# Kernel tuning notes

Measured on AMD Instinct MI355X. Metric: run time of the kernel, lower is better.

Reference implementation:

```python
import jax, jax.numpy as jnp
import numpy as np

N = 50000      # nodes
E = 800000     # edges (before self-loops)
F_IN = 256     # num_features
H = 4          # heads
C = 64         # hidden_channels
HC = H * C     # 256
L = 2          # n_layers
G = 128        # num graphs
DENSE = 64     # dense_nhid
NCLS = 2       # num_classes
NEG_SLOPE = 0.2
BN_EPS = 1e-5


def setup_inputs() -> dict:
    key = jax.random.key(0)
    ks = jax.random.split(key, 16)
    s = 0.1
    inp = {}
    inp['x'] = jax.random.normal(ks[0], (N, F_IN), jnp.float32)
    inp['edge_index'] = jax.random.randint(ks[1], (2, E), 0, N, dtype=jnp.int32)
    inp['batch'] = jnp.sort(jax.random.randint(ks[2], (N,), 0, G, dtype=jnp.int32))
    # conv1 (GATConv: lin weight [in, H*C], att vectors [H, C], bias [H*C])
    inp['W1'] = jax.random.normal(ks[3], (F_IN, HC), jnp.float32) * s
    inp['as1'] = jax.random.normal(ks[4], (H, C), jnp.float32) * s
    inp['ad1'] = jax.random.normal(ks[5], (H, C), jnp.float32) * s
    inp['b1'] = jnp.zeros((HC,), jnp.float32)
    # stacked params for the L inner conv layers + their BatchNorms
    inp['Wl'] = jax.random.normal(ks[6], (L, HC, HC), jnp.float32) * s
    inp['asl'] = jax.random.normal(ks[7], (L, H, C), jnp.float32) * s
    inp['adl'] = jax.random.normal(ks[8], (L, H, C), jnp.float32) * s
    inp['bl'] = jnp.zeros((L, HC), jnp.float32)
    inp['bng'] = jnp.ones((L, HC), jnp.float32)
    inp['bnb'] = jnp.zeros((L, HC), jnp.float32)
    # bn1 + MLP head
    inp['bn1g'] = jnp.ones((HC,), jnp.float32)
    inp['bn1b'] = jnp.zeros((HC,), jnp.float32)
    inp['lin1W'] = jax.random.normal(ks[9], (HC, DENSE), jnp.float32) * s
    inp['lin1b'] = jnp.zeros((DENSE,), jnp.float32)
    inp['lin2W'] = jax.random.normal(ks[10], (DENSE, DENSE), jnp.float32) * s
    inp['lin2b'] = jnp.zeros((DENSE,), jnp.float32)
    inp['lin3W'] = jax.random.normal(ks[11], (DENSE, NCLS), jnp.float32) * s
    inp['lin3b'] = jnp.zeros((NCLS,), jnp.float32)
    return inp


def _gat(x, src, dst, W, a_src, a_dst, b):
    # GATConv: h_j = W x_j; e_ij = LeakyReLU(a_src.h_j + a_dst.h_i);
    # alpha = softmax over incoming edges of node i; out_i = sum_j alpha*h_j (concat heads) + bias
    h = (x @ W).reshape(-1, H, C)                       # [N, H, C]
    es = jnp.sum(h * a_src, axis=-1)                    # [N, H]
    ed = jnp.sum(h * a_dst, axis=-1)                    # [N, H]
    e = jax.nn.leaky_relu(es[src] + ed[dst], NEG_SLOPE) # [E2, H]
    m = jax.ops.segment_max(e, dst, num_segments=N)
    ex = jnp.exp(e - m[dst])
    ssum = jax.ops.segment_sum(ex, dst, num_segments=N)
    alpha = ex / (ssum[dst] + 1e-16)                    # [E2, H]
    agg = jax.ops.segment_sum(h[src] * alpha[:, :, None], dst, num_segments=N)
    return agg.reshape(-1, HC) + b


def _bn(x, g, b):
    # BatchNorm1d in training mode (biased batch variance)
    mu = jnp.mean(x, axis=0)
    var = jnp.mean((x - mu) ** 2, axis=0)
    return (x - mu) / jnp.sqrt(var + BN_EPS) * g + b


def reference(x, edge_index, batch, W1, as1, ad1, b1, Wl, asl, adl, bl, bng, bnb,
              bn1g, bn1b, lin1W, lin1b, lin2W, lin2b, lin3W, lin3b):
    loops = jnp.arange(N, dtype=edge_index.dtype)
    src = jnp.concatenate([edge_index[0], loops])  # GATConv adds self-loops
    dst = jnp.concatenate([edge_index[1], loops])
    h = jax.nn.relu(_gat(x, src, dst, W1, as1, ad1, b1))
    for i in range(L):
        h = jax.nn.relu(_bn(_gat(h, src, dst, Wl[i], asl[i], adl[i], bl[i]), bng[i], bnb[i]))
    cnt = jax.ops.segment_sum(jnp.ones((N,), h.dtype), batch, num_segments=G)
    pooled = jax.ops.segment_sum(h, batch, num_segments=G) / jnp.maximum(cnt, 1.0)[:, None]
    z = _bn(pooled, bn1g, bn1b)  # dropout is identity in eval
    z = jax.nn.relu(z @ lin1W + lin1b)
    z = jax.nn.relu(z @ lin2W + lin2b)
    z = jax.nn.relu(z @ lin3W + lin3b)
    out = jax.nn.softmax(z, axis=1)
    return (out, pooled)
```

## Files before the change

### kernel.cpp

```cpp
#include <hip/hip_runtime.h>

#define N_NODES 50000
#define E_EDGES 800000
#define E2 (E_EDGES + N_NODES)
#define HC 256
#define NHEAD 4
#define GG 128
#define DENSE 64
#define NCLS 2
#define BN_EPS 1e-5f
#define NEG_SLOPE 0.2f
#define NEG_BIG -1e30f

typedef __attribute__((ext_vector_type(8))) short bf16x8;
typedef __attribute__((ext_vector_type(4))) float f32x4;

__device__ __forceinline__ unsigned short f2bf(float f) {
    unsigned int u = __float_as_uint(f);
    u = (u + 0x7FFFu + ((u >> 16) & 1u)) >> 16;
    return (unsigned short)u;
}
__device__ __forceinline__ float bf2f(unsigned short h) {
    return __uint_as_float(((unsigned int)h) << 16);
}
__device__ __forceinline__ float lrelu(float e) {
    return (e >= 0.f) ? e : NEG_SLOPE * e;
}
__device__ __forceinline__ void accum8(float acc[8], uint4 v, float w) {
    acc[0] = fmaf(w, __uint_as_float(v.x << 16), acc[0]);
    acc[1] = fmaf(w, __uint_as_float(v.x & 0xffff0000u), acc[1]);
    acc[2] = fmaf(w, __uint_as_float(v.y << 16), acc[2]);
    acc[3] = fmaf(w, __uint_as_float(v.y & 0xffff0000u), acc[3]);
    acc[4] = fmaf(w, __uint_as_float(v.z << 16), acc[4]);
    acc[5] = fmaf(w, __uint_as_float(v.z & 0xffff0000u), acc[5]);
    acc[6] = fmaf(w, __uint_as_float(v.w << 16), acc[6]);
    acc[7] = fmaf(w, __uint_as_float(v.w & 0xffff0000u), acc[7]);
}

__global__ __launch_bounds__(256) void convert_bf16_kernel(const float* __restrict__ in,
                                                           unsigned short* __restrict__ out,
                                                           int n8) {
    int i = blockIdx.x * blockDim.x + threadIdx.x;
    if (i >= n8) return;
    const float4* p = reinterpret_cast<const float4*>(in + (size_t)i * 8);
    float4 a = p[0], b = p[1];
    ushort4 lo = make_ushort4(f2bf(a.x), f2bf(a.y), f2bf(a.z), f2bf(a.w));
    ushort4 hi = make_ushort4(f2bf(b.x), f2bf(b.y), f2bf(b.z), f2bf(b.w));
    ushort4* q = reinterpret_cast<ushort4*>(out + (size_t)i * 8);
    q[0] = lo; q[1] = hi;
}

__global__ __launch_bounds__(64) void pack_b_kernel(const float* __restrict__ W,
                                                    unsigned short* __restrict__ Bpk) {
    int l = threadIdx.x;
    int g = blockIdx.x;
    int ks = g >> 4, ct = g & 15;
    int col = ct * 16 + (l & 15);
    int k0 = ks * 32 + (l >> 4) * 8;
    unsigned short v[8];
#pragma unroll
    for (int j = 0; j < 8; ++j) v[j] = f2bf(W[(size_t)(k0 + j) * HC + col]);
    ushort4* q = reinterpret_cast<ushort4*>(Bpk + ((size_t)g * 64 + l) * 8);
    q[0] = make_ushort4(v[0], v[1], v[2], v[3]);
    q[1] = make_ushort4(v[4], v[5], v[6], v[7]);
}

__global__ __launch_bounds__(256) void gemm_mfma_kernel(const unsigned short* __restrict__ A,
                                                        const unsigned short* __restrict__ Bpk,
                                                        const float* __restrict__ prm,
                                                        unsigned short* __restrict__ C, int M) {
    __shared__ unsigned short As[64 * 256];
    int tid = threadIdx.x;
    int lane = tid & 63, wid = tid >> 6;
    int row0 = blockIdx.x * 64;
#pragma unroll
    for (int i = 0; i < 8; ++i) {
        int idx = tid + i * 256;
        int row = idx >> 5, c16 = idx & 31;
        int grow = row0 + row;
        uint4 v = make_uint4(0u, 0u, 0u, 0u);
        if (grow < M) v = *reinterpret_cast<const uint4*>(A + (size_t)grow * HC + c16 * 8);
        if (prm) {
            int ch = c16 * 8;
            const float4 s0 = *reinterpret_cast<const float4*>(prm + ch);
            const float4 s1 = *reinterpret_cast<const float4*>(prm + ch + 4);
            const float4 t0 = *reinterpret_cast<const float4*>(prm + HC + ch);
            const float4 t1 = *reinterpret_cast<const float4*>(prm + HC + ch + 4);
            float f0 = fmaxf(fmaf(__uint_as_float(v.x << 16),          s0.x, t0.x), 0.f);
            float f1 = fmaxf(fmaf(__uint_as_float(v.x & 0xffff0000u),  s0.y, t0.y), 0.f);
            float f2 = fmaxf(fmaf(__uint_as_float(v.y << 16),          s0.z, t0.z), 0.f);
            float f3 = fmaxf(fmaf(__uint_as_float(v.y & 0xffff0000u),  s0.w, t0.w), 0.f);
            float f4 = fmaxf(fmaf(__uint_as_float(v.z << 16),          s1.x, t1.x), 0.f);
            float f5 = fmaxf(fmaf(__uint_as_float(v.z & 0xffff0000u),  s1.y, t1.y), 0.f);
            float f6 = fmaxf(fmaf(__uint_as_float(v.w << 16),          s1.z, t1.z), 0.f);
            float f7 = fmaxf(fmaf(__uint_as_float(v.w & 0xffff0000u),  s1.w, t1.w), 0.f);
            v.x = (unsigned int)f2bf(f0) | ((unsigned int)f2bf(f1) << 16);
            v.y = (unsigned int)f2bf(f2) | ((unsigned int)f2bf(f3) << 16);
            v.z = (unsigned int)f2bf(f4) | ((unsigned int)f2bf(f5) << 16);
            v.w = (unsigned int)f2bf(f6) | ((unsigned int)f2bf(f7) << 16);
        }
        int byteoff = row * 512 + c16 * 16;
        byteoff ^= (row & 7) << 4;
        *reinterpret_cast<uint4*>((char*)As + byteoff) = v;
    }
    __syncthreads();

    f32x4 acc[16];
#pragma unroll
    for (int ct = 0; ct < 16; ++ct) acc[ct] = (f32x4){0.f, 0.f, 0.f, 0.f};

    int mrow = wid * 16 + (lane & 15);
#pragma unroll
    for (int ks = 0; ks < 8; ++ks) {
        int abyte = mrow * 512 + ks * 64 + (lane >> 4) * 16;
        abyte ^= (mrow & 7) << 4;
        bf16x8 a = *reinterpret_cast<const bf16x8*>((char*)As + abyte);
        const unsigned short* bp = Bpk + ((size_t)(ks * 16) * 512 + lane * 8);
#pragma unroll
        for (int ct = 0; ct < 16; ++ct) {
            bf16x8 b = *reinterpret_cast<const bf16x8*>(bp + (size_t)ct * 512);
            acc[ct] = __builtin_amdgcn_mfma_f32_16x16x32_bf16(a, b, acc[ct], 0, 0, 0);
        }
    }
    int crow0 = row0 + wid * 16 + (lane >> 4) * 4;
    int ccol = lane & 15;
#pragma unroll
    for (int ct = 0; ct < 16; ++ct) {
#pragma unroll
        for (int r = 0; r < 4; ++r) {
            int grow = crow0 + r;
            if (grow < M) C[(size_t)grow * HC + ct * 16 + ccol] = f2bf(acc[ct][r]);
        }
    }
}

__global__ __launch_bounds__(256) void esed_kernel(const unsigned short* __restrict__ h,
                                                   const float* __restrict__ avs,
                                                   const float* __restrict__ avd,
                                                   float* __restrict__ es, float* __restrict__ ed) {
    int tid = threadIdx.x;
    int lane = tid & 63, wid = tid >> 6;
    int node = blockIdx.x * 4 + wid;
    if (node >= N_NODES) return;
    int ch0 = lane * 4;
    ushort4 hv = *reinterpret_cast<const ushort4*>(h + (size_t)node * HC + ch0);
    float4 sa = *reinterpret_cast<const float4*>(avs + ch0);
    float4 da = *reinterpret_cast<const float4*>(avd + ch0);
    float h0 = bf2f(hv.x), h1 = bf2f(hv.y), h2 = bf2f(hv.z), h3 = bf2f(hv.w);
    float vs = h0 * sa.x + h1 * sa.y + h2 * sa.z + h3 * sa.w;
    float vd = h0 * da.x + h1 * da.y + h2 * da.z + h3 * da.w;
#pragma unroll
    for (int m = 1; m < 16; m <<= 1) {
        vs += __shfl_xor(vs, m, 64);
        vd += __shfl_xor(vd, m, 64);
    }
    if ((lane & 15) == 0) {
        es[node * NHEAD + (lane >> 4)] = vs;
        ed[node * NHEAD + (lane >> 4)] = vd;
    }
}

__global__ void init_deg_kernel(int* __restrict__ deg) {
    int i = blockIdx.x * blockDim.x + threadIdx.x;
    if (i < N_NODES) deg[i] = 1;
}
__global__ void count_edges_kernel(const int* __restrict__ dst, int* __restrict__ deg) {
    int i = blockIdx.x * blockDim.x + threadIdx.x;
    if (i < E_EDGES) atomicAdd(&deg[dst[i]], 1);
}
__global__ __launch_bounds__(1024) void scan1_kernel(const int* __restrict__ deg,
                                                     int* __restrict__ rs, int* __restrict__ bsum) {
    __shared__ int wsum[16];
    int t = threadIdx.x, lane = t & 63, wid = t >> 6;
    int i = blockIdx.x * 1024 + t;
    int v = (i < N_NODES) ? deg[i] : 0;
    int x = v;
#pragma unroll
    for (int off = 1; off < 64; off <<= 1) {
        int y = __shfl_up(x, off, 64);
        if (lane >= off) x += y;
    }
    if (lane == 63) wsum[wid] = x;
    __syncthreads();
    if (wid == 0) {
        int s = (lane < 16) ? wsum[lane] : 0;
#pragma unroll
        for (int off = 1; off < 16; off <<= 1) {
            int y = __shfl_up(s, off, 64);
            if (lane >= off) s += y;
        }
        if (lane < 16) wsum[lane] = s;
    }
    __syncthreads();
    int woff = wid ? wsum[wid - 1] : 0;
    if (i <= N_NODES) rs[i] = woff + x - v;
    if (t == 1023) bsum[blockIdx.x] = wsum[15];
}
__global__ void scan2_kernel(int* __restrict__ bsum, int nb) {
    int l = threadIdx.x;
    int v = (l < nb) ? bsum[l] : 0;
    int x = v;
#pragma unroll
    for (int off = 1; off < 64; off <<= 1) {
        int y = __shfl_up(x, off, 64);
        if (l >= off) x += y;
    }
    if (l < nb) bsum[l] = x - v;
}
__global__ void scan3_kernel(int* __restrict__ rs, const int* __restrict__ bsum,
                             int* __restrict__ cursor, int* __restrict__ csr) {
    int i = blockIdx.x * blockDim.x + threadIdx.x;
    if (i <= N_NODES) {
        int v = rs[i] + bsum[i >> 10];
        rs[i] = v;
        if (i < N_NODES) {
            csr[v] = i;
            cursor[i] = v + 1;
        }
    }
}
__global__ void scatter_edges_kernel(const int* __restrict__ src, const int* __restrict__ dst,
                                     int* __restrict__ cursor, int* __restrict__ csr) {
    int i = blockIdx.x * blockDim.x + threadIdx.x;
    if (i < E_EDGES) {
        int pos = atomicAdd(&cursor[dst[i]], 1);
        csr[pos] = src[i];
    }
}

__global__ __launch_bounds__(256) void smprep_kernel(const float* __restrict__ es,
                                                     const float* __restrict__ ed,
                                                     const int* __restrict__ rs,
                                                     const int* __restrict__ csr,
                                                     float* __restrict__ alpha) {
    int tid = threadIdx.x;
    int lane = tid & 63, wid = tid >> 6;
    int node = blockIdx.x * 4 + wid;
    if (node >= N_NODES) return;
    int head = lane >> 4, slot = lane & 15;
    float edn = ed[node * NHEAD + head];
    int beg = rs[node], end = rs[node + 1];
    float m = NEG_BIG, s = 0.f;
    for (int i = beg + slot; i < end; i += 16) {
        float e = lrelu(es[csr[i] * NHEAD + head] + edn);
        alpha[(size_t)i * NHEAD + head] = e;
        float mn = fmaxf(m, e);
        s = s * __expf(m - mn) + __expf(e - mn);
        m = mn;
    }
#pragma unroll
    for (int off = 1; off < 16; off <<= 1) {
        float mo = __shfl_xor(m, off, 64);
        float so = __shfl_xor(s, off, 64);
        float mn = fmaxf(m, mo);
        s = s * __expf(m - mn) + so * __expf(mo - mn);
        m = mn;
    }
    float inv = 1.f / (s + 1e-16f);
    for (int i = beg + slot; i < end; i += 16) {
        float e = alpha[(size_t)i * NHEAD + head];
        alpha[(size_t)i * NHEAD + head] = __expf(e - m) * inv;
    }
}

__global__ __launch_bounds__(256) void gat_agg_kernel(const unsigned short* __restrict__ hlin,
                                                      const float* __restrict__ alpha,
                                                      const int* __restrict__ rs,
                                                      const int* __restrict__ csr,
                                                      const float* __restrict__ bias,
                                                      unsigned short* __restrict__ out, int do_relu) {
    int tid = threadIdx.x;
    int lane = tid & 63, wid = tid >> 6;
    int node = blockIdx.x * 8 + wid * 2 + (lane >> 5);
    int hl = lane & 31;
    int ch0 = hl * 8;
    int head = hl >> 3;
    bool valid = node < N_NODES;
    int beg = valid ? rs[node] : 0;
    int end = valid ? rs[node + 1] : 0;
    float acc[8] = {};
    int idx = beg;
    for (; idx + 8 <= end; idx += 8) {
        int si[8]; float pi[8];
#pragma unroll
        for (int j = 0; j < 8; ++j) {
            si[j] = csr[idx + j];
            pi[j] = alpha[(size_t)(idx + j) * NHEAD + head];
        }
        uint4 v[8];
#pragma unroll
        for (int j = 0; j < 8; ++j)
            v[j] = *reinterpret_cast<const uint4*>(hlin + (size_t)si[j] * HC + ch0);
#pragma unroll
        for (int j = 0; j < 8; ++j) accum8(acc, v[j], pi[j]);
    }
    if (idx + 4 <= end) {
        int s0 = csr[idx], s1 = csr[idx + 1], s2 = csr[idx + 2], s3 = csr[idx + 3];
        float p0 = alpha[(size_t)idx * NHEAD + head];
        float p1 = alpha[(size_t)(idx + 1) * NHEAD + head];
        float p2 = alpha[(size_t)(idx + 2) * NHEAD + head];
        float p3 = alpha[(size_t)(idx + 3) * NHEAD + head];
        uint4 v0 = *reinterpret_cast<const uint4*>(hlin + (size_t)s0 * HC + ch0);
        uint4 v1 = *reinterpret_cast<const uint4*>(hlin + (size_t)s1 * HC + ch0);
        uint4 v2 = *reinterpret_cast<const uint4*>(hlin + (size_t)s2 * HC + ch0);
        uint4 v3 = *reinterpret_cast<const uint4*>(hlin + (size_t)s3 * HC + ch0);
        accum8(acc, v0, p0);
        accum8(acc, v1, p1);
        accum8(acc, v2, p2);
        accum8(acc, v3, p3);
        idx += 4;
    }
    for (; idx < end; ++idx) {
        int s0 = csr[idx];
        float p0 = alpha[(size_t)idx * NHEAD + head];
        uint4 v0 = *reinterpret_cast<const uint4*>(hlin + (size_t)s0 * HC + ch0);
        accum8(acc, v0, p0);
    }
    if (!valid) return;
    const float4 bva = *reinterpret_cast<const float4*>(bias + ch0);
    const float4 bvb = *reinterpret_cast<const float4*>(bias + ch0 + 4);
    float o[8];
    o[0] = acc[0] + bva.x; o[1] = acc[1] + bva.y; o[2] = acc[2] + bva.z; o[3] = acc[3] + bva.w;
    o[4] = acc[4] + bvb.x; o[5] = acc[5] + bvb.y; o[6] = acc[6] + bvb.z; o[7] = acc[7] + bvb.w;
    if (do_relu) {
#pragma unroll
        for (int j = 0; j < 8; ++j) o[j] = fmaxf(o[j], 0.f);
    }
    uint4 w;
    w.x = (unsigned int)f2bf(o[0]) | ((unsigned int)f2bf(o[1]) << 16);
    w.y = (unsigned int)f2bf(o[2]) | ((unsigned int)f2bf(o[3]) << 16);
    w.z = (unsigned int)f2bf(o[4]) | ((unsigned int)f2bf(o[5]) << 16);
    w.w = (unsigned int)f2bf(o[6]) | ((unsigned int)f2bf(o[7]) << 16);
    *reinterpret_cast<uint4*>(out + (size_t)node * HC + ch0) = w;
}

#define BN_RPB 49
__global__ __launch_bounds__(256) void bn_stats_kernel(const unsigned short* __restrict__ x,
                                                       float* __restrict__ sums) {
    __shared__ float lds[8][512];
    int tid = threadIdx.x;
    int c = tid & 31;
    int rt = tid >> 5;
    int r0 = blockIdx.x * BN_RPB;
    int r1 = min(N_NODES, r0 + BN_RPB);
    int ch = c * 8;
    float s[8] = {}, s2[8] = {};
    for (int r = r0 + rt; r < r1; r += 8) {
        const ushort4* p = reinterpret_cast<const ushort4*>(x + (size_t)r * HC + ch);
        ushort4 va = p[0], vb = p[1];
        unsigned short in[8] = {va.x, va.y, va.z, va.w, vb.x, vb.y, vb.z, vb.w};
#pragma unroll
        for (int j = 0; j < 8; ++j) {
            float v = bf2f(in[j]);
            s[j] += v; s2[j] += v * v;
        }
    }
#pragma unroll
    for (int j = 0; j < 8; ++j) {
        lds[rt][ch + j] = s[j];
        lds[rt][256 + ch + j] = s2[j];
    }
    __syncthreads();
#pragma unroll
    for (int e = tid; e < 512; e += 256) {
        float v = 0.f;
#pragma unroll
        for (int r = 0; r < 8; ++r) v += lds[r][e];
        atomicAdd(&sums[e], v);
    }
}
__global__ void bn_finalize_kernel(const float* __restrict__ sums, const float* __restrict__ g,
                                   const float* __restrict__ b, float* __restrict__ prm) {
    int t = threadIdx.x;
    float mean = sums[t] / (float)N_NODES;
    float var = sums[HC + t] / (float)N_NODES - mean * mean;
    var = fmaxf(var, 0.f);
    float scale = g[t] * rsqrtf(var + BN_EPS);
    prm[t] = scale;
    prm[HC + t] = b[t] - mean * scale;
}

__global__ __launch_bounds__(GG) void graph_ub_kernel(const int* __restrict__ batch,
                                                      int* __restrict__ ub) {
    int g = threadIdx.x;
    int lo = 0, hi = N_NODES;
    while (lo < hi) {
        int mid = (lo + hi) >> 1;
        if (batch[mid] <= g) lo = mid + 1; else hi = mid;
    }
    ub[g] = lo;
}
#define POOL_RPB 32
__global__ __launch_bounds__(256) void pool_kernel(const unsigned short* __restrict__ h,
                                                   const float* __restrict__ prm,
                                                   const int* __restrict__ batch,
                                                   float* __restrict__ psum) {
    int tid = threadIdx.x;
    int ct = tid & 63;
    int rt = tid >> 6;
    int r0 = blockIdx.x * POOL_RPB;
    int r1 = min(N_NODES, r0 + POOL_RPB);
    int ch = ct * 4;
    const float4 sc = *reinterpret_cast<const float4*>(prm + ch);
    const float4 sh = *reinterpret_cast<const float4*>(prm + HC + ch);
    float a0 = 0.f, a1 = 0.f, a2 = 0.f, a3 = 0.f;
    int gcur = -1;
    for (int r = r0 + rt; r < r1; r += 4) {
        int g = batch[r];
        if (g != gcur) {
            if (gcur >= 0) {
                atomicAdd(&psum[gcur * HC + ch + 0], a0);
                atomicAdd(&psum[gcur * HC + ch + 1], a1);
                atomicAdd(&psum[gcur * HC + ch + 2], a2);
                atomicAdd(&psum[gcur * HC + ch + 3], a3);
            }
            a0 = a1 = a2 = a3 = 0.f; gcur = g;
        }
        ushort4 hv = *reinterpret_cast<const ushort4*>(h + (size_t)r * HC + ch);
        a0 += fmaxf(fmaf(bf2f(hv.x), sc.x, sh.x), 0.f);
        a1 += fmaxf(fmaf(bf2f(hv.y), sc.y, sh.y), 0.f);
        a2 += fmaxf(fmaf(bf2f(hv.z), sc.z, sh.z), 0.f);
        a3 += fmaxf(fmaf(bf2f(hv.w), sc.w, sh.w), 0.f);
    }
    if (gcur >= 0) {
        atomicAdd(&psum[gcur * HC + ch + 0], a0);
        atomicAdd(&psum[gcur * HC + ch + 1], a1);
        atomicAdd(&psum[gcur * HC + ch + 2], a2);
        atomicAdd(&psum[gcur * HC + ch + 3], a3);
    }
}
__global__ void pool_fin_kernel(const float* __restrict__ psum, const int* __restrict__ ub,
                                float* __restrict__ pooled) {
    int g = blockIdx.x, t = threadIdx.x;
    int c = ub[g] - (g > 0 ? ub[g - 1] : 0);
    float cf = fmaxf((float)c, 1.f);
    pooled[g * HC + t] = psum[g * HC + t] / cf;
}

__global__ __launch_bounds__(256) void bn_head_kernel(const float* __restrict__ pooled,
                                                      const float* __restrict__ g,
                                                      const float* __restrict__ b,
                                                      float* __restrict__ z) {
    int t = threadIdx.x;
    float s = 0.f, s2 = 0.f;
    for (int r = 0; r < GG; ++r) {
        float v = pooled[r * HC + t];
        s += v; s2 += v * v;
    }
    float mean = s / (float)GG;
    float var = fmaxf(s2 / (float)GG - mean * mean, 0.f);
    float scale = g[t] * rsqrtf(var + BN_EPS);
    float shift = b[t] - mean * scale;
    for (int r = 0; r < GG; ++r)
        z[r * HC + t] = pooled[r * HC + t] * scale + shift;
}
__global__ __launch_bounds__(64) void lin_relu_kernel(const float* __restrict__ X,
                                                      const float* __restrict__ W,
                                                      const float* __restrict__ b,
                                                      float* __restrict__ Y, int K) {
    __shared__ float xr[256];
    int r = blockIdx.x, t = threadIdx.x;
    for (int k = t; k < K; k += 64) xr[k] = X[r * K + k];
    __syncthreads();
    float a = b[t];
    for (int k = 0; k < K; ++k) a += xr[k] * W[k * DENSE + t];
    Y[r * DENSE + t] = fmaxf(a, 0.f);
}
__global__ __launch_bounds__(128) void lin3_softmax_kernel(const float* __restrict__ X,
                                                           const float* __restrict__ W,
                                                           const float* __restrict__ b,
                                                           float* __restrict__ out) {
    int r = threadIdx.x;
    const float* xr = X + r * DENSE;
    float o0 = b[0], o1 = b[1];
    for (int k = 0; k < DENSE; ++k) {
        o0 += xr[k] * W[k * NCLS + 0];
        o1 += xr[k] * W[k * NCLS + 1];
    }
    o0 = fmaxf(o0, 0.f); o1 = fmaxf(o1, 0.f);
    float mx = fmaxf(o0, o1);
    float e0 = __expf(o0 - mx), e1 = __expf(o1 - mx);
    float inv = 1.f / (e0 + e1);
    out[r * NCLS + 0] = e0 * inv;
    out[r * NCLS + 1] = e1 * inv;
}

extern "C" void kernel_launch(void* const* d_in, const int* in_sizes, int n_in,
                              void* d_out, int out_size, void* d_ws, size_t ws_size,
                              hipStream_t stream) {
    const float* x     = (const float*)d_in[0];
    const int*   ei    = (const int*)d_in[1];
    const int*   srcp  = ei;
    const int*   dstp  = ei + E_EDGES;
    const int*   batch = (const int*)d_in[2];
    const float* W1    = (const float*)d_in[3];
    const float* as1   = (const float*)d_in[4];
    const float* ad1   = (const float*)d_in[5];
    const float* b1    = (const float*)d_in[6];
    const float* Wl    = (const float*)d_in[7];
    const float* asl   = (const float*)d_in[8];
    const float* adl   = (const float*)d_in[9];
    const float* bl    = (const float*)d_in[10];
    const float* bng   = (const float*)d_in[11];
    const float* bnb   = (const float*)d_in[12];
    const float* bn1g  = (const float*)d_in[13];
    const float* bn1b  = (const float*)d_in[14];
    const float* l1W   = (const float*)d_in[15];
    const float* l1b   = (const float*)d_in[16];
    const float* l2W   = (const float*)d_in[17];
    const float* l2b   = (const float*)d_in[18];
    const float* l3W   = (const float*)d_in[19];
    const float* l3b   = (const float*)d_in[20];

    float* outp   = (float*)d_out;
    float* pooled = outp + GG * NCLS;

    char* w = (char*)d_ws;
    auto alloc = [&](size_t bytes) -> void* {
        void* p = (void*)w;
        w += (bytes + 255) & ~(size_t)255;
        return p;
    };
    unsigned short* xb  = (unsigned short*)alloc(sizeof(short) * (size_t)N_NODES * HC);
    unsigned short* h0  = (unsigned short*)alloc(sizeof(short) * (size_t)N_NODES * HC);
    unsigned short* h1  = (unsigned short*)alloc(sizeof(short) * (size_t)N_NODES * HC);
    unsigned short* h2  = (unsigned short*)alloc(sizeof(short) * (size_t)N_NODES * HC);
    unsigned short* Bpk = (unsigned short*)alloc(sizeof(short) * 3 * 128 * 64 * 8);
    float* es     = (float*)alloc(sizeof(float) * (size_t)N_NODES * NHEAD);
    float* ed     = (float*)alloc(sizeof(float) * (size_t)N_NODES * NHEAD);
    float* alpha  = (float*)alloc(sizeof(float) * (size_t)E2 * NHEAD);
    int*   rs     = (int*)alloc(sizeof(int) * (N_NODES + 1));
    int*   deg    = (int*)alloc(sizeof(int) * N_NODES);
    int*   csr    = (int*)alloc(sizeof(int) * E2);
    int*   bsum   = (int*)alloc(sizeof(int) * 64);
    float* bnsums = (float*)alloc(sizeof(float) * 2 * HC);
    float* bnprm  = (float*)alloc(sizeof(float) * 2 * HC);
    float* psum   = (float*)alloc(sizeof(float) * GG * HC);
    int*   ub     = (int*)alloc(sizeof(int) * GG);
    float* z0     = (float*)alloc(sizeof(float) * GG * HC);
    float* z1     = (float*)alloc(sizeof(float) * GG * DENSE);
    float* z2     = (float*)alloc(sizeof(float) * GG * DENSE);

    const int nblk_nodes = (N_NODES + 255) / 256;
    const int nblk_edges = (E_EDGES + 255) / 256;
    const int nblk_wave4 = (N_NODES + 3) / 4;
    const int nblk_wave8 = (N_NODES + 7) / 8;
    const int nscan = (N_NODES + 1023) / 1024;
    const int nblk_bn   = (N_NODES + BN_RPB - 1) / BN_RPB;
    const int nblk_pool = (N_NODES + POOL_RPB - 1) / POOL_RPB;

    pack_b_kernel<<<128, 64, 0, stream>>>(W1, Bpk);
    pack_b_kernel<<<128, 64, 0, stream>>>(Wl, Bpk + 128 * 64 * 8);
    pack_b_kernel<<<128, 64, 0, stream>>>(Wl + (size_t)HC * HC, Bpk + 2 * 128 * 64 * 8);
    convert_bf16_kernel<<<(N_NODES * HC / 8 + 255) / 256, 256, 0, stream>>>(x, xb, N_NODES * HC / 8);

    init_deg_kernel<<<nblk_nodes, 256, 0, stream>>>(deg);
    count_edges_kernel<<<nblk_edges, 256, 0, stream>>>(dstp, deg);
    scan1_kernel<<<nscan, 1024, 0, stream>>>(deg, rs, bsum);
    scan2_kernel<<<1, 64, 0, stream>>>(bsum, nscan);
    scan3_kernel<<<(N_NODES + 256) / 256, 256, 0, stream>>>(rs, bsum, deg, csr);
    scatter_edges_kernel<<<nblk_edges, 256, 0, stream>>>(srcp, dstp, deg, csr);

    const int ggrid = (N_NODES + 63) / 64;

    gemm_mfma_kernel<<<ggrid, 256, 0, stream>>>(xb, Bpk, nullptr, h1, N_NODES);
    esed_kernel<<<nblk_wave4, 256, 0, stream>>>(h1, as1, ad1, es, ed);
    smprep_kernel<<<nblk_wave4, 256, 0, stream>>>(es, ed, rs, csr, alpha);
    gat_agg_kernel<<<nblk_wave8, 256, 0, stream>>>(h1, alpha, rs, csr, b1, h0, 1);

    gemm_mfma_kernel<<<ggrid, 256, 0, stream>>>(h0, Bpk + 128 * 64 * 8, nullptr, h1, N_NODES);
    esed_kernel<<<nblk_wave4, 256, 0, stream>>>(h1, asl, adl, es, ed);
    smprep_kernel<<<nblk_wave4, 256, 0, stream>>>(es, ed, rs, csr, alpha);
    gat_agg_kernel<<<nblk_wave8, 256, 0, stream>>>(h1, alpha, rs, csr, bl, h2, 0);
    hipMemsetAsync(bnsums, 0, sizeof(float) * 2 * HC, stream);
    bn_stats_kernel<<<nblk_bn, 256, 0, stream>>>(h2, bnsums);
    bn_finalize_kernel<<<1, 256, 0, stream>>>(bnsums, bng, bnb, bnprm);

    gemm_mfma_kernel<<<ggrid, 256, 0, stream>>>(h2, Bpk + 2 * 128 * 64 * 8, bnprm, h1, N_NODES);
    esed_kernel<<<nblk_wave4, 256, 0, stream>>>(h1, asl + HC, adl + HC, es, ed);
    smprep_kernel<<<nblk_wave4, 256, 0, stream>>>(es, ed, rs, csr, alpha);
    gat_agg_kernel<<<nblk_wave8, 256, 0, stream>>>(h1, alpha, rs, csr, bl + HC, h2, 0);
    hipMemsetAsync(bnsums, 0, sizeof(float) * 2 * HC, stream);
    bn_stats_kernel<<<nblk_bn, 256, 0, stream>>>(h2, bnsums);
    bn_finalize_kernel<<<1, 256, 0, stream>>>(bnsums, bng + HC, bnb + HC, bnprm);

    hipMemsetAsync(psum, 0, sizeof(float) * GG * HC, stream);
    graph_ub_kernel<<<1, GG, 0, stream>>>(batch, ub);
    pool_kernel<<<nblk_pool, 256, 0, stream>>>(h2, bnprm, batch, psum);
    pool_fin_kernel<<<GG, HC, 0, stream>>>(psum, ub, pooled);

    bn_head_kernel<<<1, HC, 0, stream>>>(pooled, bn1g, bn1b, z0);
    lin_relu_kernel<<<GG, 64, 0, stream>>>(z0, l1W, l1b, z1, HC);
    lin_relu_kernel<<<GG, 64, 0, stream>>>(z1, l2W, l2b, z2, DENSE);
    lin3_softmax_kernel<<<1, GG, 0, stream>>>(z2, l3W, l3b, outp);
}
```

Measured before the change: 607.0 us.

## Fuse input conversion and attention scores into GEMM, merge small kernels

The fp32-to-bf16 conversion of x now happens in the first GEMM's A-tile load, and the per-node attention dot products (es/ed) are computed in the GEMM epilogue from fp32 accumulators. This drops the convert and esed kernels and one full read of h per layer. The three weight-pack launches become one, and the graph upper-bound kernel is folded into pool_fin as a per-block binary search. The gather loop in gat_agg is cut from 8-wide to 4-wide unrolling, which lowers register pressure but also reduces memory-level parallelism. The es/ed values now come from unrounded accumulators rather than bf16-rounded h, a small numeric difference.

```diff
diff --git a/kernel.cpp b/kernel.cpp
--- a/kernel.cpp
+++ b/kernel.cpp
@@ -37,38 +37,33 @@
     acc[7] = fmaf(w, __uint_as_float(v.w & 0xffff0000u), acc[7]);
 }
 
-__global__ __launch_bounds__(256) void convert_bf16_kernel(const float* __restrict__ in,
-                                                           unsigned short* __restrict__ out,
-                                                           int n8) {
-    int i = blockIdx.x * blockDim.x + threadIdx.x;
-    if (i >= n8) return;
-    const float4* p = reinterpret_cast<const float4*>(in + (size_t)i * 8);
-    float4 a = p[0], b = p[1];
-    ushort4 lo = make_ushort4(f2bf(a.x), f2bf(a.y), f2bf(a.z), f2bf(a.w));
-    ushort4 hi = make_ushort4(f2bf(b.x), f2bf(b.y), f2bf(b.z), f2bf(b.w));
-    ushort4* q = reinterpret_cast<ushort4*>(out + (size_t)i * 8);
-    q[0] = lo; q[1] = hi;
-}
-
-__global__ __launch_bounds__(64) void pack_b_kernel(const float* __restrict__ W,
+__global__ __launch_bounds__(64) void pack_b_kernel(const float* __restrict__ W1,
+                                                    const float* __restrict__ Wl,
                                                     unsigned short* __restrict__ Bpk) {
     int l = threadIdx.x;
-    int g = blockIdx.x;
+    int mat = blockIdx.x >> 7;
+    int g = blockIdx.x & 127;
+    const float* W = (mat == 0) ? W1 : Wl + (size_t)(mat - 1) * HC * HC;
     int ks = g >> 4, ct = g & 15;
     int col = ct * 16 + (l & 15);
     int k0 = ks * 32 + (l >> 4) * 8;
     unsigned short v[8];
 #pragma unroll
     for (int j = 0; j < 8; ++j) v[j] = f2bf(W[(size_t)(k0 + j) * HC + col]);
-    ushort4* q = reinterpret_cast<ushort4*>(Bpk + ((size_t)g * 64 + l) * 8);
+    ushort4* q = reinterpret_cast<ushort4*>(Bpk + ((size_t)mat * 128 * 512) + ((size_t)g * 64 + l) * 8);
     q[0] = make_ushort4(v[0], v[1], v[2], v[3]);
     q[1] = make_ushort4(v[4], v[5], v[6], v[7]);
 }
 
 __global__ __launch_bounds__(256) void gemm_mfma_kernel(const unsigned short* __restrict__ A,
+                                                        const float* __restrict__ A32,
                                                         const unsigned short* __restrict__ Bpk,
                                                         const float* __restrict__ prm,
-                                                        unsigned short* __restrict__ C, int M) {
+                                                        const float* __restrict__ avs,
+                                                        const float* __restrict__ avd,
+                                                        unsigned short* __restrict__ C,
+                                                        float* __restrict__ es,
+                                                        float* __restrict__ ed, int M) {
     __shared__ unsigned short As[64 * 256];
     int tid = threadIdx.x;
     int lane = tid & 63, wid = tid >> 6;
@@ -79,25 +74,36 @@
         int row = idx >> 5, c16 = idx & 31;
         int grow = row0 + row;
         uint4 v = make_uint4(0u, 0u, 0u, 0u);
-        if (grow < M) v = *reinterpret_cast<const uint4*>(A + (size_t)grow * HC + c16 * 8);
-        if (prm) {
-            int ch = c16 * 8;
-            const float4 s0 = *reinterpret_cast<const float4*>(prm + ch);
-            const float4 s1 = *reinterpret_cast<const float4*>(prm + ch + 4);
-            const float4 t0 = *reinterpret_cast<const float4*>(prm + HC + ch);
-            const float4 t1 = *reinterpret_cast<const float4*>(prm + HC + ch + 4);
-            float f0 = fmaxf(fmaf(__uint_as_float(v.x << 16),          s0.x, t0.x), 0.f);
-            float f1 = fmaxf(fmaf(__uint_as_float(v.x & 0xffff0000u),  s0.y, t0.y), 0.f);
-            float f2 = fmaxf(fmaf(__uint_as_float(v.y << 16),          s0.z, t0.z), 0.f);
-            float f3 = fmaxf(fmaf(__uint_as_float(v.y & 0xffff0000u),  s0.w, t0.w), 0.f);
-            float f4 = fmaxf(fmaf(__uint_as_float(v.z << 16),          s1.x, t1.x), 0.f);
-            float f5 = fmaxf(fmaf(__uint_as_float(v.z & 0xffff0000u),  s1.y, t1.y), 0.f);
-            float f6 = fmaxf(fmaf(__uint_as_float(v.w << 16),          s1.z, t1.z), 0.f);
-            float f7 = fmaxf(fmaf(__uint_as_float(v.w & 0xffff0000u),  s1.w, t1.w), 0.f);
-            v.x = (unsigned int)f2bf(f0) | ((unsigned int)f2bf(f1) << 16);
-            v.y = (unsigned int)f2bf(f2) | ((unsigned int)f2bf(f3) << 16);
-            v.z = (unsigned int)f2bf(f4) | ((unsigned int)f2bf(f5) << 16);
-            v.w = (unsigned int)f2bf(f6) | ((unsigned int)f2bf(f7) << 16);
+        if (A32) {
+            if (grow < M) {
+                const float4* p = reinterpret_cast<const float4*>(A32 + (size_t)grow * HC + c16 * 8);
+                float4 a = p[0], b = p[1];
+                v.x = (unsigned int)f2bf(a.x) | ((unsigned int)f2bf(a.y) << 16);
+                v.y = (unsigned int)f2bf(a.z) | ((unsigned int)f2bf(a.w) << 16);
+                v.z = (unsigned int)f2bf(b.x) | ((unsigned int)f2bf(b.y) << 16);
+                v.w = (unsigned int)f2bf(b.z) | ((unsigned int)f2bf(b.w) << 16);
+            }
+        } else {
+            if (grow < M) v = *reinterpret_cast<const uint4*>(A + (size_t)grow * HC + c16 * 8);
+            if (prm) {
+                int ch = c16 * 8;
+                const float4 s0 = *reinterpret_cast<const float4*>(prm + ch);
+                const float4 s1 = *reinterpret_cast<const float4*>(prm + ch + 4);
+                const float4 t0 = *reinterpret_cast<const float4*>(prm + HC + ch);
+                const float4 t1 = *reinterpret_cast<const float4*>(prm + HC + ch + 4);
+                float f0 = fmaxf(fmaf(__uint_as_float(v.x << 16),          s0.x, t0.x), 0.f);
+                float f1 = fmaxf(fmaf(__uint_as_float(v.x & 0xffff0000u),  s0.y, t0.y), 0.f);
+                float f2 = fmaxf(fmaf(__uint_as_float(v.y << 16),          s0.z, t0.z), 0.f);
+                float f3 = fmaxf(fmaf(__uint_as_float(v.y & 0xffff0000u),  s0.w, t0.w), 0.f);
+                float f4 = fmaxf(fmaf(__uint_as_float(v.z << 16),          s1.x, t1.x), 0.f);
+                float f5 = fmaxf(fmaf(__uint_as_float(v.z & 0xffff0000u),  s1.y, t1.y), 0.f);
+                float f6 = fmaxf(fmaf(__uint_as_float(v.w << 16),          s1.z, t1.z), 0.f);
+                float f7 = fmaxf(fmaf(__uint_as_float(v.w & 0xffff0000u),  s1.w, t1.w), 0.f);
+                v.x = (unsigned int)f2bf(f0) | ((unsigned int)f2bf(f1) << 16);
+                v.y = (unsigned int)f2bf(f2) | ((unsigned int)f2bf(f3) << 16);
+                v.z = (unsigned int)f2bf(f4) | ((unsigned int)f2bf(f5) << 16);
+                v.w = (unsigned int)f2bf(f6) | ((unsigned int)f2bf(f7) << 16);
+            }
         }
         int byteoff = row * 512 + c16 * 16;
         byteoff ^= (row & 7) << 4;
@@ -132,31 +138,34 @@
             if (grow < M) C[(size_t)grow * HC + ct * 16 + ccol] = f2bf(acc[ct][r]);
         }
     }
-}
-
-__global__ __launch_bounds__(256) void esed_kernel(const unsigned short* __restrict__ h,
-                                                   const float* __restrict__ avs,
-                                                   const float* __restrict__ avd,
-                                                   float* __restrict__ es, float* __restrict__ ed) {
-    int tid = threadIdx.x;
-    int lane = tid & 63, wid = tid >> 6;
-    int node = blockIdx.x * 4 + wid;
-    if (node >= N_NODES) return;
-    int ch0 = lane * 4;
-    ushort4 hv = *reinterpret_cast<const ushort4*>(h + (size_t)node * HC + ch0);
-    float4 sa = *reinterpret_cast<const float4*>(avs + ch0);
-    float4 da = *reinterpret_cast<const float4*>(avd + ch0);
-    float h0 = bf2f(hv.x), h1 = bf2f(hv.y), h2 = bf2f(hv.z), h3 = bf2f(hv.w);
-    float vs = h0 * sa.x + h1 * sa.y + h2 * sa.z + h3 * sa.w;
-    float vd = h0 * da.x + h1 * da.y + h2 * da.z + h3 * da.w;
-#pragma unroll
-    for (int m = 1; m < 16; m <<= 1) {
-        vs += __shfl_xor(vs, m, 64);
-        vd += __shfl_xor(vd, m, 64);
-    }
-    if ((lane & 15) == 0) {
-        es[node * NHEAD + (lane >> 4)] = vs;
-        ed[node * NHEAD + (lane >> 4)] = vd;
+    float avsv[16], advv[16];
+#pragma unroll
+    for (int ct = 0; ct < 16; ++ct) {
+        avsv[ct] = avs[ct * 16 + ccol];
+        advv[ct] = avd[ct * 16 + ccol];
+    }
+#pragma unroll
+    for (int r = 0; r < 4; ++r) {
+        int grow = crow0 + r;
+        float p0 = acc[0][r]*avsv[0] + acc[1][r]*avsv[1] + acc[2][r]*avsv[2] + acc[3][r]*avsv[3];
+        float p1 = acc[4][r]*avsv[4] + acc[5][r]*avsv[5] + acc[6][r]*avsv[6] + acc[7][r]*avsv[7];
+        float p2 = acc[8][r]*avsv[8] + acc[9][r]*avsv[9] + acc[10][r]*avsv[10] + acc[11][r]*avsv[11];
+        float p3 = acc[12][r]*avsv[12] + acc[13][r]*avsv[13] + acc[14][r]*avsv[14] + acc[15][r]*avsv[15];
+        float q0 = acc[0][r]*advv[0] + acc[1][r]*advv[1] + acc[2][r]*advv[2] + acc[3][r]*advv[3];
+        float q1 = acc[4][r]*advv[4] + acc[5][r]*advv[5] + acc[6][r]*advv[6] + acc[7][r]*advv[7];
+        float q2 = acc[8][r]*advv[8] + acc[9][r]*advv[9] + acc[10][r]*advv[10] + acc[11][r]*advv[11];
+        float q3 = acc[12][r]*advv[12] + acc[13][r]*advv[13] + acc[14][r]*advv[14] + acc[15][r]*advv[15];
+#pragma unroll
+        for (int off = 1; off < 16; off <<= 1) {
+            p0 += __shfl_xor(p0, off, 64); p1 += __shfl_xor(p1, off, 64);
+            p2 += __shfl_xor(p2, off, 64); p3 += __shfl_xor(p3, off, 64);
+            q0 += __shfl_xor(q0, off, 64); q1 += __shfl_xor(q1, off, 64);
+            q2 += __shfl_xor(q2, off, 64); q3 += __shfl_xor(q3, off, 64);
+        }
+        if (ccol == 0 && grow < M) {
+            *reinterpret_cast<float4*>(es + (size_t)grow * 4) = make_float4(p0, p1, p2, p3);
+            *reinterpret_cast<float4*>(ed + (size_t)grow * 4) = make_float4(q0, q1, q2, q3);
+        }
     }
 }
 
@@ -280,21 +289,7 @@
     int end = valid ? rs[node + 1] : 0;
     float acc[8] = {};
     int idx = beg;
-    for (; idx + 8 <= end; idx += 8) {
-        int si[8]; float pi[8];
-#pragma unroll
-        for (int j = 0; j < 8; ++j) {
-            si[j] = csr[idx + j];
-            pi[j] = alpha[(size_t)(idx + j) * NHEAD + head];
-        }
-        uint4 v[8];
-#pragma unroll
-        for (int j = 0; j < 8; ++j)
-            v[j] = *reinterpret_cast<const uint4*>(hlin + (size_t)si[j] * HC + ch0);
-#pragma unroll
-        for (int j = 0; j < 8; ++j) accum8(acc, v[j], pi[j]);
-    }
-    if (idx + 4 <= end) {
+    for (; idx + 4 <= end; idx += 4) {
         int s0 = csr[idx], s1 = csr[idx + 1], s2 = csr[idx + 2], s3 = csr[idx + 3];
         float p0 = alpha[(size_t)idx * NHEAD + head];
         float p1 = alpha[(size_t)(idx + 1) * NHEAD + head];
@@ -308,7 +303,6 @@
         accum8(acc, v1, p1);
         accum8(acc, v2, p2);
         accum8(acc, v3, p3);
-        idx += 4;
     }
     for (; idx < end; ++idx) {
         int s0 = csr[idx];
@@ -380,16 +374,6 @@
     prm[HC + t] = b[t] - mean * scale;
 }
 
-__global__ __launch_bounds__(GG) void graph_ub_kernel(const int* __restrict__ batch,
-                                                      int* __restrict__ ub) {
-    int g = threadIdx.x;
-    int lo = 0, hi = N_NODES;
-    while (lo < hi) {
-        int mid = (lo + hi) >> 1;
-        if (batch[mid] <= g) lo = mid + 1; else hi = mid;
-    }
-    ub[g] = lo;
-}
 #define POOL_RPB 32
 __global__ __launch_bounds__(256) void pool_kernel(const unsigned short* __restrict__ h,
                                                    const float* __restrict__ prm,
@@ -429,11 +413,14 @@
         atomicAdd(&psum[gcur * HC + ch + 3], a3);
     }
 }
-__global__ void pool_fin_kernel(const float* __restrict__ psum, const int* __restrict__ ub,
+__global__ void pool_fin_kernel(const float* __restrict__ psum, const int* __restrict__ batch,
                                 float* __restrict__ pooled) {
     int g = blockIdx.x, t = threadIdx.x;
-    int c = ub[g] - (g > 0 ? ub[g - 1] : 0);
-    float cf = fmaxf((float)c, 1.f);
+    int lo = 0, hi = N_NODES;
+    while (lo < hi) { int mid = (lo + hi) >> 1; if (batch[mid] <= g) lo = mid + 1; else hi = mid; }
+    int lo2 = 0, hi2 = N_NODES;
+    while (lo2 < hi2) { int mid = (lo2 + hi2) >> 1; if (batch[mid] <= g - 1) lo2 = mid + 1; else hi2 = mid; }
+    float cf = fmaxf((float)(lo - lo2), 1.f);
     pooled[g * HC + t] = psum[g * HC + t] / cf;
 }
 
@@ -521,7 +508,6 @@
         w += (bytes + 255) & ~(size_t)255;
         return p;
     };
-    unsigned short* xb  = (unsigned short*)alloc(sizeof(short) * (size_t)N_NODES * HC);
     unsigned short* h0  = (unsigned short*)alloc(sizeof(short) * (size_t)N_NODES * HC);
     unsigned short* h1  = (unsigned short*)alloc(sizeof(short) * (size_t)N_NODES * HC);
     unsigned short* h2  = (unsigned short*)alloc(sizeof(short) * (size_t)N_NODES * HC);
@@ -536,7 +522,6 @@
     float* bnsums = (float*)alloc(sizeof(float) * 2 * HC);
     float* bnprm  = (float*)alloc(sizeof(float) * 2 * HC);
     float* psum   = (float*)alloc(sizeof(float) * GG * HC);
-    int*   ub     = (int*)alloc(sizeof(int) * GG);
     float* z0     = (float*)alloc(sizeof(float) * GG * HC);
     float* z1     = (float*)alloc(sizeof(float) * GG * DENSE);
     float* z2     = (float*)alloc(sizeof(float) * GG * DENSE);
@@ -549,10 +534,7 @@
     const int nblk_bn   = (N_NODES + BN_RPB - 1) / BN_RPB;
     const int nblk_pool = (N_NODES + POOL_RPB - 1) / POOL_RPB;
 
-    pack_b_kernel<<<128, 64, 0, stream>>>(W1, Bpk);
-    pack_b_kernel<<<128, 64, 0, stream>>>(Wl, Bpk + 128 * 64 * 8);
-    pack_b_kernel<<<128, 64, 0, stream>>>(Wl + (size_t)HC * HC, Bpk + 2 * 128 * 64 * 8);
-    convert_bf16_kernel<<<(N_NODES * HC / 8 + 255) / 256, 256, 0, stream>>>(x, xb, N_NODES * HC / 8);
+    pack_b_kernel<<<384, 64, 0, stream>>>(W1, Wl, Bpk);
 
     init_deg_kernel<<<nblk_nodes, 256, 0, stream>>>(deg);
     count_edges_kernel<<<nblk_edges, 256, 0, stream>>>(dstp, deg);
@@ -563,21 +545,18 @@
 
     const int ggrid = (N_NODES + 63) / 64;
 
-    gemm_mfma_kernel<<<ggrid, 256, 0, stream>>>(xb, Bpk, nullptr, h1, N_NODES);
-    esed_kernel<<<nblk_wave4, 256, 0, stream>>>(h1, as1, ad1, es, ed);
+    gemm_mfma_kernel<<<ggrid, 256, 0, stream>>>(nullptr, x, Bpk, nullptr, as1, ad1, h1, es, ed, N_NODES);
     smprep_kernel<<<nblk_wave4, 256, 0, stream>>>(es, ed, rs, csr, alpha);
     gat_agg_kernel<<<nblk_wave8, 256, 0, stream>>>(h1, alpha, rs, csr, b1, h0, 1);
 
-    gemm_mfma_kernel<<<ggrid, 256, 0, stream>>>(h0, Bpk + 128 * 64 * 8, nullptr, h1, N_NODES);
-    esed_kernel<<<nblk_wave4, 256, 0, stream>>>(h1, asl, adl, es, ed);
+    gemm_mfma_kernel<<<ggrid, 256, 0, stream>>>(h0, nullptr, Bpk + 128 * 512, nullptr, asl, adl, h1, es, ed, N_NODES);
     smprep_kernel<<<nblk_wave4, 256, 0, stream>>>(es, ed, rs, csr, alpha);
     gat_agg_kernel<<<nblk_wave8, 256, 0, stream>>>(h1, alpha, rs, csr, bl, h2, 0);
     hipMemsetAsync(bnsums, 0, sizeof(float) * 2 * HC, stream);
     bn_stats_kernel<<<nblk_bn, 256, 0, stream>>>(h2, bnsums);
     bn_finalize_kernel<<<1, 256, 0, stream>>>(bnsums, bng, bnb, bnprm);
 
-    gemm_mfma_kernel<<<ggrid, 256, 0, stream>>>(h2, Bpk + 2 * 128 * 64 * 8, bnprm, h1, N_NODES);
-    esed_kernel<<<nblk_wave4, 256, 0, stream>>>(h1, asl + HC, adl + HC, es, ed);
+    gemm_mfma_kernel<<<ggrid, 256, 0, stream>>>(h2, nullptr, Bpk + 2 * 128 * 512, bnprm, asl + HC, adl + HC, h1, es, ed, N_NODES);
     smprep_kernel<<<nblk_wave4, 256, 0, stream>>>(es, ed, rs, csr, alpha);
     gat_agg_kernel<<<nblk_wave8, 256, 0, stream>>>(h1, alpha, rs, csr, bl + HC, h2, 0);
     hipMemsetAsync(bnsums, 0, sizeof(float) * 2 * HC, stream);
@@ -585,9 +564,8 @@
     bn_finalize_kernel<<<1, 256, 0, stream>>>(bnsums, bng + HC, bnb + HC, bnprm);
 
     hipMemsetAsync(psum, 0, sizeof(float) * GG * HC, stream);
-    graph_ub_kernel<<<1, GG, 0, stream>>>(batch, ub);
     pool_kernel<<<nblk_pool, 256, 0, stream>>>(h2, bnprm, batch, psum);
-    pool_fin_kernel<<<GG, HC, 0, stream>>>(psum, ub, pooled);
+    pool_fin_kernel<<<GG, HC, 0, stream>>>(psum, batch, pooled);
 
     bn_head_kernel<<<1, HC, 0, stream>>>(pooled, bn1g, bn1b, z0);
     lin_relu_kernel<<<GG, 64, 0, stream>>>(z0, l1W, l1b, z1, HC);
```

Result: no change. 615.8 us (+1.4%).
